# Performance work log

Hardware: AMD Instinct MI355X
Metric: run time of the kernel (lower is better)

## Reference

```python
import jax, jax.numpy as jnp
import numpy as np
from jax.ops import segment_sum

N_NODES = 100000

def setup_inputs() -> dict:
    key = jax.random.key(0)
    k1, k2, k3 = jax.random.split(key, 3)
    x = jax.random.normal(k1, (N_NODES, 128), dtype=jnp.float32)
    edge_weight = jax.random.uniform(k2, (3200000,), dtype=jnp.float32)
    edge_index = jax.random.randint(k3, (2, 3200000), 0, N_NODES, dtype=jnp.int64)
    return {"x": x, "edge_weight": edge_weight, "edge_index": edge_index}

def reference(x, edge_weight, edge_index):
    # GCNConv with weight forced to identity (in==out channels, no bias):
    # lin(x) == x, so the op is gcn_norm + scatter-add aggregation.
    n = x.shape[0]
    # add self loops with fill value 1.0 (improved=False)
    loop_idx = jnp.arange(n, dtype=edge_index.dtype)
    row = jnp.concatenate([edge_index[0], loop_idx])
    col = jnp.concatenate([edge_index[1], loop_idx])
    ew = jnp.concatenate([edge_weight, jnp.ones((n,), dtype=edge_weight.dtype)])
    # symmetric normalization: deg computed at target (col)
    deg = segment_sum(ew, col, num_segments=n)
    dinv = jnp.where(deg > 0, jax.lax.rsqrt(deg), 0.0)
    norm = dinv[row] * ew * dinv[col]
    # message = norm * x[src]; aggregate (sum) at target
    msgs = x[row] * norm[:, None]          # [E+N, d]
    out = segment_sum(msgs, col, num_segments=n)  # [N, d]
    return out
```

## Files before the change

kernel.cpp:

```cpp
#include <hip/hip_runtime.h>
#include <hip/hip_fp16.h>
#include <math.h>

#define FEAT      128
#define PITCH     72
#define CH        6144
#define K_EDGES   12
#define MAXBINS   512
#define CAP_MAX   9216
#define K2        18

__global__ void conv_xs_kernel(const float* __restrict__ x,
                               const float* __restrict__ dinv,
                               __half2* __restrict__ xs, int n4) {
    int i = blockIdx.x * blockDim.x + threadIdx.x;
    if (i >= n4) return;
    float s = dinv[i >> 5];
    float4 v = ((const float4*)x)[i];
    xs[2 * i]     = __floats2half2_rn(s * v.x, s * v.y);
    xs[2 * i + 1] = __floats2half2_rn(s * v.z, s * v.w);
}

__global__ __launch_bounds__(512) void p1_partition_kernel(
        const int* __restrict__ row,
        const int* __restrict__ col,
        const float* __restrict__ ew,
        int* __restrict__ bin_cursor,
        unsigned long long* __restrict__ binned,
        int E, int NBINS, int cap) {
    __shared__ unsigned long long stage[CH];
    __shared__ int hist[MAXBINS];
    __shared__ int lofs[MAXBINS];
    __shared__ int lcnt[MAXBINS];
    __shared__ int gbase[MAXBINS];
    __shared__ int scanbuf[MAXBINS];
    int tid = threadIdx.x;
    if (tid < MAXBINS) { hist[tid] = 0; lcnt[tid] = 0; }
    __syncthreads();

    int start = blockIdx.x * CH;
    int end   = start + CH; if (end > E) end = E;
    int total = end - start;

    unsigned long long ed[K_EDGES];
    int ebin[K_EDGES];
    #pragma unroll
    for (int k = 0; k < K_EDGES; k++) {
        int e = start + (k << 9) + tid;
        if (e < end) {
            int c = col[e];
            unsigned short wh = __half_as_ushort(__float2half_rn(ew[e]));
            ed[k] = ((unsigned long long)wh << 48)
                  | ((unsigned long long)((unsigned)row[e] & 0xFFFFFFu) << 24)
                  | (unsigned)(c & 0xFFFFFFu);
            ebin[k] = c >> 8;
            atomicAdd(&hist[ebin[k]], 1);
        } else {
            ebin[k] = -1;
        }
    }
    __syncthreads();

    int h = (tid < NBINS) ? hist[tid] : 0;
    scanbuf[tid] = h;
    __syncthreads();
    #pragma unroll
    for (int off = 1; off < MAXBINS; off <<= 1) {
        int t = (tid >= off) ? scanbuf[tid - off] : 0;
        __syncthreads();
        scanbuf[tid] += t;
        __syncthreads();
    }
    lofs[tid] = scanbuf[tid] - h;
    __syncthreads();

    #pragma unroll
    for (int k = 0; k < K_EDGES; k++) {
        if (ebin[k] >= 0) {
            int pos = lofs[ebin[k]] + atomicAdd(&lcnt[ebin[k]], 1);
            stage[pos] = ed[k];
        }
    }
    if (tid < NBINS)
        gbase[tid] = hist[tid] ? atomicAdd(&bin_cursor[tid], hist[tid]) : 0;
    __syncthreads();

    for (int i = tid; i < total; i += 512) {
        unsigned long long e = stage[i];
        int bin = (int)((e >> 8) & 0xFFFFu);
        int pos = gbase[bin] + (i - lofs[bin]);
        if (pos < cap) binned[(size_t)bin * cap + pos] = e;
    }
}

__global__ __launch_bounds__(512) void p2_build_kernel(
        const unsigned long long* __restrict__ binned,
        int* __restrict__ bin_cursor,
        unsigned long long* __restrict__ csr,
        float* __restrict__ dinv,
        int* __restrict__ countg,
        const float* __restrict__ x,
        __half2* __restrict__ xs,
        int N, int NBINS, int cap) {
    __shared__ unsigned long long stage[CAP_MAX];
    __shared__ float degf[256];
    __shared__ int cnt[256];
    __shared__ int pfx[256];
    __shared__ int lcnt[256];
    __shared__ float sdi[256];
    __shared__ int wsum[4];
    __shared__ int binBase_s;
    int tid = threadIdx.x;
    if (tid < 256) { degf[tid] = 0.0f; cnt[tid] = 0; lcnt[tid] = 0; }
    __syncthreads();

    int b = blockIdx.x;
    int nE = bin_cursor[b]; if (nE > cap) nE = cap;
    const unsigned long long* src = binned + (size_t)b * cap;
    int nodeBase = b << 8;

    unsigned long long ed[K2];
    #pragma unroll
    for (int k = 0; k < K2; k++) {
        int i = tid + (k << 9);
        if (i < nE) {
            unsigned long long p = src[i];
            int cl     = (int)(p & 255u);
            unsigned r = (unsigned)((p >> 24) & 0xFFFFFFu);
            float w = __half2float(__ushort_as_half((unsigned short)(p >> 48)));
            atomicAdd(&cnt[cl], 1);
            atomicAdd(&degf[cl], w);
            ed[k] = ((unsigned long long)__float_as_uint(w) << 32)
                  | ((unsigned)cl << 24) | r;
        }
    }
    if (tid == 0) binBase_s = atomicAdd(&bin_cursor[NBINS], nE);
    __syncthreads();

    if (tid < 256) {
        int w = tid >> 6, l = tid & 63;
        int v = cnt[tid];
        int inc = v;
        #pragma unroll
        for (int d = 1; d < 64; d <<= 1) {
            int t = __shfl_up(inc, d);
            if (l >= d) inc += t;
        }
        if (l == 63) wsum[w] = inc;
        pfx[tid] = inc - v;
    }
    __syncthreads();
    if (tid < 256) {
        int w = tid >> 6;
        int add = 0;
        for (int q = 0; q < w; q++) add += wsum[q];
        pfx[tid] += add;
    }
    __syncthreads();

    #pragma unroll
    for (int k = 0; k < K2; k++) {
        int i = tid + (k << 9);
        if (i < nE) {
            unsigned long long p = ed[k];
            int cl = (int)((p >> 24) & 255u);
            int slot = atomicAdd(&lcnt[cl], 1);
            stage[pfx[cl] + slot] = p & 0xFFFFFFFF00FFFFFFULL;
        }
    }
    __syncthreads();

    int binBase = binBase_s;
    for (int i = tid; i < nE; i += 512)
        csr[(size_t)binBase + i] = stage[i];
    if (tid < 256) {
        int node = nodeBase + tid;
        if (node < N) {
            float di = rsqrtf(1.0f + degf[tid]);
            sdi[tid] = di;
            dinv[node] = di;
            int c2 = cnt[tid]; if (c2 > 255) c2 = 255;
            countg[node] = (int)((((unsigned)(binBase + pfx[tid])) << 8) | (unsigned)c2);
        } else {
            sdi[tid] = 0.0f;
        }
    }
    __syncthreads();

    int nValid = N - nodeBase; if (nValid > 256) nValid = 256;
    if (nValid > 0) {
        int total4 = nValid << 5;
        for (int idx = tid; idx < total4; idx += 512) {
            int cl = idx >> 5;
            float s = sdi[cl];
            size_t g = ((size_t)(nodeBase + cl) << 5) + (idx & 31);
            float4 v = ((const float4*)x)[g];
            xs[2 * g]     = __floats2half2_rn(s * v.x, s * v.y);
            xs[2 * g + 1] = __floats2half2_rn(s * v.z, s * v.w);
        }
    }
}

#define GLD(q)  unsigned long long p##q = eb[wid][j + q];               \
                unsigned r##q = (unsigned)p##q;                          \
                float w##q = __uint_as_float((unsigned)(p##q >> 32));    \
                __half2 h##q = xs[(r##q << 6) | lane];
#define GFMA(q, acc)  { float2 v##q = __half22float2(h##q);              \
                acc.x = fmaf(w##q, v##q.x, acc.x);                       \
                acc.y = fmaf(w##q, v##q.y, acc.y); }

__global__ __launch_bounds__(256) void gather_xs_kernel(
        const __half2* __restrict__ xs,
        const float* __restrict__ dinv,
        const int* __restrict__ countg,
        const unsigned long long* __restrict__ csr,
        float* __restrict__ out, int nodeBase, int nEnd) {
    __shared__ unsigned long long eb[4][64];
    int wid  = threadIdx.x >> 6;
    int node = nodeBase + blockIdx.x * 4 + wid;
    int lane = threadIdx.x & 63;
    if (node >= nEnd) return;

    float di = dinv[node];
    unsigned c = (unsigned)countg[node];
    int cnt = (int)(c & 255u);
    const unsigned long long* b = csr + (c >> 8);

    unsigned long long e0 = (lane < cnt) ? b[lane] : 0ULL;
    eb[wid][lane] = e0;

    unsigned xbase = ((unsigned)node << 6) | (unsigned)lane;
    float2 xv = __half22float2(xs[xbase]);
    float2 a0 = xv;
    float2 a1 = {0.f, 0.f}, a2 = {0.f, 0.f}, a3 = {0.f, 0.f};

    int m = cnt < 64 ? cnt : 64;
    int j = 0;
    for (; j + 16 <= m; j += 16) {
        GLD(0)  GLD(1)  GLD(2)  GLD(3)  GLD(4)  GLD(5)  GLD(6)  GLD(7)
        GLD(8)  GLD(9)  GLD(10) GLD(11) GLD(12) GLD(13) GLD(14) GLD(15)
        GFMA(0, a0)  GFMA(1, a1)  GFMA(2, a2)  GFMA(3, a3)
        GFMA(4, a0)  GFMA(5, a1)  GFMA(6, a2)  GFMA(7, a3)
        GFMA(8, a0)  GFMA(9, a1)  GFMA(10, a2) GFMA(11, a3)
        GFMA(12, a0) GFMA(13, a1) GFMA(14, a2) GFMA(15, a3)
    }
    for (; j + 8 <= m; j += 8) {
        GLD(0)  GLD(1)  GLD(2)  GLD(3)  GLD(4)  GLD(5)  GLD(6)  GLD(7)
        GFMA(0, a0)  GFMA(1, a1)  GFMA(2, a2)  GFMA(3, a3)
        GFMA(4, a0)  GFMA(5, a1)  GFMA(6, a2)  GFMA(7, a3)
    }
    for (; j + 4 <= m; j += 4) {
        GLD(0)  GLD(1)  GLD(2)  GLD(3)
        GFMA(0, a0)  GFMA(1, a1)  GFMA(2, a2)  GFMA(3, a3)
    }
    for (; j < m; ++j) {
        GLD(0)
        GFMA(0, a0)
    }
    for (; j < cnt; ++j) {
        unsigned long long p0 = b[j];
        unsigned r0 = (unsigned)p0;
        float w0 = __uint_as_float((unsigned)(p0 >> 32));
        float2 v0 = __half22float2(xs[(r0 << 6) | lane]);
        a0.x = fmaf(w0, v0.x, a0.x);  a0.y = fmaf(w0, v0.y, a0.y);
    }
    float2 r;
    r.x = di * ((a0.x + a1.x) + (a2.x + a3.x));
    r.y = di * ((a0.y + a1.y) + (a2.y + a3.y));
    ((float2*)(out + (size_t)node * FEAT))[lane] = r;
}


__global__ void init_packed_kernel(unsigned long long* __restrict__ packed, int n) {
    int i = blockIdx.x * blockDim.x + threadIdx.x;
    if (i < n) packed[i] = (1ULL << 32);
}

__global__ void passA_kernel(const int* __restrict__ row,
                             const int* __restrict__ col,
                             const float* __restrict__ ew,
                             unsigned long long* __restrict__ packed,
                             unsigned long long* __restrict__ bucket, int E) {
    int e = blockIdx.x * blockDim.x + threadIdx.x;
    if (e >= E) return;
    int c = col[e], r = row[e];
    float w = ew[e];
    unsigned long long v = (1ULL << 40)
        | (unsigned long long)((double)w * 4294967296.0);
    unsigned long long old = atomicAdd(&packed[c], v);
    unsigned int slot = (unsigned int)(old >> 40);
    if (slot < PITCH)
        bucket[(size_t)c * PITCH + slot] =
            ((unsigned long long)__float_as_uint(w) << 32) | ((unsigned int)r & 0xFFFFFFu);
}

__global__ void make_dinv_count_kernel(const unsigned long long* __restrict__ packed,
                                       float* __restrict__ dinv,
                                       int* __restrict__ countg, int n) {
    int i = blockIdx.x * blockDim.x + threadIdx.x;
    if (i < n) {
        unsigned long long p = packed[i];
        unsigned long long frac = p & ((1ULL << 40) - 1);
        float d = (float)((double)frac * (1.0 / 4294967296.0));
        dinv[i] = rsqrtf(d);
        int c = (int)(p >> 40); if (c > PITCH) c = PITCH;
        countg[i] = (int)((((unsigned)i * (unsigned)PITCH) << 8) | (unsigned)c);
    }
}


__global__ void init_deg_kernel(float* __restrict__ deg, int n) {
    int i = blockIdx.x * blockDim.x + threadIdx.x;
    if (i < n) deg[i] = 1.0f;
}
__global__ void deg_accum_kernel(const int* __restrict__ col,
                                 const float* __restrict__ ew,
                                 float* __restrict__ deg, int E) {
    int e = blockIdx.x * blockDim.x + threadIdx.x;
    if (e < E) atomicAdd(&deg[col[e]], ew[e]);
}
__global__ void make_dinv_kernel(const float* __restrict__ deg,
                                 float* __restrict__ dinv, int n) {
    int i = blockIdx.x * blockDim.x + threadIdx.x;
    if (i < n) {
        float d = deg[i];
        dinv[i] = d > 0.0f ? rsqrtf(d) : 0.0f;
    }
}
__global__ void init_out_kernel(const float* __restrict__ x,
                                const float* __restrict__ dinv,
                                float* __restrict__ out, int n) {
    int idx = blockIdx.x * blockDim.x + threadIdx.x;
    int i = idx >> 5, lane = idx & 31;
    if (i >= n) return;
    float s = dinv[i] * dinv[i];
    float4 v = ((const float4*)(x + (size_t)i * FEAT))[lane];
    float4 r;
    r.x = s * v.x; r.y = s * v.y; r.z = s * v.z; r.w = s * v.w;
    ((float4*)(out + (size_t)i * FEAT))[lane] = r;
}
__global__ void scatter_kernel(const float* __restrict__ x,
                               const float* __restrict__ ew,
                               const int* __restrict__ row,
                               const int* __restrict__ col,
                               const float* __restrict__ dinv,
                               float* __restrict__ out, int E) {
    long long idx = (long long)blockIdx.x * blockDim.x + threadIdx.x;
    int e = (int)(idx >> 5), lane = (int)(idx & 31);
    if (e >= E) return;
    int r = row[e], c = col[e];
    float nrm = dinv[r] * ew[e] * dinv[c];
    float4 v = ((const float4*)(x + (size_t)r * FEAT))[lane];
    float* o = out + (size_t)c * FEAT + lane * 4;
    atomicAdd(o + 0, nrm * v.x);
    atomicAdd(o + 1, nrm * v.y);
    atomicAdd(o + 2, nrm * v.z);
    atomicAdd(o + 3, nrm * v.w);
}


static inline size_t align256(size_t v) { return (v + 255) & ~(size_t)255; }

extern "C" void kernel_launch(void* const* d_in, const int* in_sizes, int n_in,
                              void* d_out, int out_size, void* d_ws, size_t ws_size,
                              hipStream_t stream) {
    const float* x  = (const float*)d_in[0];
    const float* ew = (const float*)d_in[1];
    const int*   ei = (const int*)d_in[2];

    const int N = in_sizes[0] / FEAT;
    const int E = in_sizes[1];
    const int* row = ei;
    const int* col = ei + E;

    float* out = (float*)d_out;
    const int B = 256;
    char* w = (char*)d_ws;

    const int NBINS = (N + 255) >> 8;
    const int avg   = (E + NBINS - 1) / NBINS;
    int cap = avg + 8 * (int)sqrt((double)avg) + 64;
    if (cap > CAP_MAX) cap = CAP_MAX;

    size_t sz_csr    = align256((size_t)E * 8 + 256);
    size_t sz_bucket = align256((size_t)N * PITCH * 8);
    size_t sz_dinv   = align256((size_t)N * 4);
    size_t sz_count  = align256((size_t)N * 4);
    size_t sz_cursor = align256((size_t)(NBINS + 1) * 4);
    size_t sz_binned = align256((size_t)NBINS * (size_t)cap * 8);
    size_t sz_xs     = align256((size_t)N * FEAT * 2);

    size_t need_fast2 = sz_csr + sz_dinv + sz_count + sz_cursor + sz_binned + sz_xs;
    size_t need_fast1 = align256((size_t)N * 8) + sz_dinv + sz_count + sz_xs + sz_bucket;

    int n4 = N * FEAT / 4;

    if (ws_size >= need_fast2 && NBINS <= MAXBINS && N < (1 << 24) && E < (1 << 24)) {
        unsigned long long* csr = (unsigned long long*)w;     w += sz_csr;
        float* dinv   = (float*)w;                            w += sz_dinv;
        int*   countg = (int*)w;                              w += sz_count;
        int*   cursor = (int*)w;                              w += sz_cursor;
        unsigned long long* binned = (unsigned long long*)w;  w += sz_binned;
        __half2* xs = (__half2*)w;

        hipMemsetAsync(cursor, 0, (size_t)(NBINS + 1) * 4, stream);
        int p1b = (E + CH - 1) / CH;
        p1_partition_kernel<<<p1b, 512, 0, stream>>>(row, col, ew, cursor, binned,
                                                     E, NBINS, cap);
        p2_build_kernel<<<NBINS, 512, 0, stream>>>(binned, cursor, csr,
                                                   dinv, countg, x, xs, N, NBINS, cap);
        int q = ((N / 4) + 3) & ~3;
        for (int s4 = 0; s4 < 4; s4++) {
            int lo = q * s4;
            int hi = (s4 == 3) ? N : q * (s4 + 1);
            if (hi > lo)
                gather_xs_kernel<<<(hi - lo + 3) / 4, B, 0, stream>>>(
                    xs, dinv, countg, csr, out, lo, hi);
        }
    } else if (ws_size >= need_fast1 && N < (1 << 24) &&
               (size_t)N * PITCH < (size_t)(1 << 24)) {
        unsigned long long* packed = (unsigned long long*)w;  w += align256((size_t)N * 8);
        float*   dinv   = (float*)w;                          w += sz_dinv;
        int*     countg = (int*)w;                            w += sz_count;
        __half2* xs     = (__half2*)w;                        w += sz_xs;
        unsigned long long* bucket = (unsigned long long*)w;

        init_packed_kernel<<<(N + B - 1) / B, B, 0, stream>>>(packed, N);
        passA_kernel<<<(E + B - 1) / B, B, 0, stream>>>(row, col, ew, packed, bucket, E);
        make_dinv_count_kernel<<<(N + B - 1) / B, B, 0, stream>>>(packed, dinv, countg, N);
        conv_xs_kernel<<<(n4 + B - 1) / B, B, 0, stream>>>(x, dinv, xs, n4);
        gather_xs_kernel<<<(N + 3) / 4, B, 0, stream>>>(xs, dinv, countg, bucket, out, 0, N);
    } else {
        float* deg  = (float*)w;                  w += sz_dinv;
        float* dinv = (float*)w;
        init_deg_kernel<<<(N + B - 1) / B, B, 0, stream>>>(deg, N);
        deg_accum_kernel<<<(E + B - 1) / B, B, 0, stream>>>(col, ew, deg, E);
        make_dinv_kernel<<<(N + B - 1) / B, B, 0, stream>>>(deg, dinv, N);
        long long it = (long long)N * 32;
        init_out_kernel<<<(int)((it + B - 1) / B), B, 0, stream>>>(x, dinv, out, N);
        long long st = (long long)E * 32;
        scatter_kernel<<<(int)((st + B - 1) / B), B, 0, stream>>>(x, ew, row, col, dinv, out, E);
    }
}
```

Before: 303.7 us.

## Write CSR directly into padded per-bin slots and merge gather launches

The build kernel no longer stages edges in a 72 KB shared buffer and no longer compacts the CSR through a global atomic cursor. Each bin now writes straight into its own padded region at b*cap plus the per-node prefix, and the count/offset words are encoded against that padded layout. The cost is a second read of the binned input and scattered 8-byte global writes in place of coalesced copies, plus a larger workspace. The four partial gather launches are merged into a single launch over all nodes, removing launch overhead.

```diff
diff --git a/kernel.cpp b/kernel.cpp
--- a/kernel.cpp
+++ b/kernel.cpp
@@ -95,21 +95,19 @@
 
 __global__ __launch_bounds__(512) void p2_build_kernel(
         const unsigned long long* __restrict__ binned,
-        int* __restrict__ bin_cursor,
+        const int* __restrict__ bin_cursor,
         unsigned long long* __restrict__ csr,
         float* __restrict__ dinv,
         int* __restrict__ countg,
         const float* __restrict__ x,
         __half2* __restrict__ xs,
         int N, int NBINS, int cap) {
-    __shared__ unsigned long long stage[CAP_MAX];
     __shared__ float degf[256];
     __shared__ int cnt[256];
     __shared__ int pfx[256];
     __shared__ int lcnt[256];
     __shared__ float sdi[256];
     __shared__ int wsum[4];
-    __shared__ int binBase_s;
     int tid = threadIdx.x;
     if (tid < 256) { degf[tid] = 0.0f; cnt[tid] = 0; lcnt[tid] = 0; }
     __syncthreads();
@@ -119,22 +117,13 @@
     const unsigned long long* src = binned + (size_t)b * cap;
     int nodeBase = b << 8;
 
-    unsigned long long ed[K2];
-    #pragma unroll
-    for (int k = 0; k < K2; k++) {
-        int i = tid + (k << 9);
-        if (i < nE) {
-            unsigned long long p = src[i];
-            int cl     = (int)(p & 255u);
-            unsigned r = (unsigned)((p >> 24) & 0xFFFFFFu);
-            float w = __half2float(__ushort_as_half((unsigned short)(p >> 48)));
-            atomicAdd(&cnt[cl], 1);
-            atomicAdd(&degf[cl], w);
-            ed[k] = ((unsigned long long)__float_as_uint(w) << 32)
-                  | ((unsigned)cl << 24) | r;
-        }
-    }
-    if (tid == 0) binBase_s = atomicAdd(&bin_cursor[NBINS], nE);
+    for (int i = tid; i < nE; i += 512) {
+        unsigned long long p = src[i];
+        int cl = (int)(p & 255u);
+        float w = __half2float(__ushort_as_half((unsigned short)(p >> 48)));
+        atomicAdd(&cnt[cl], 1);
+        atomicAdd(&degf[cl], w);
+    }
     __syncthreads();
 
     if (tid < 256) {
@@ -154,38 +143,31 @@
         int w = tid >> 6;
         int add = 0;
         for (int q = 0; q < w; q++) add += wsum[q];
-        pfx[tid] += add;
-    }
-    __syncthreads();
-
-    #pragma unroll
-    for (int k = 0; k < K2; k++) {
-        int i = tid + (k << 9);
-        if (i < nE) {
-            unsigned long long p = ed[k];
-            int cl = (int)((p >> 24) & 255u);
-            int slot = atomicAdd(&lcnt[cl], 1);
-            stage[pfx[cl] + slot] = p & 0xFFFFFFFF00FFFFFFULL;
-        }
-    }
-    __syncthreads();
-
-    int binBase = binBase_s;
-    for (int i = tid; i < nE; i += 512)
-        csr[(size_t)binBase + i] = stage[i];
-    if (tid < 256) {
+        int p = pfx[tid] + add;
+        pfx[tid] = p;
         int node = nodeBase + tid;
         if (node < N) {
             float di = rsqrtf(1.0f + degf[tid]);
             sdi[tid] = di;
             dinv[node] = di;
             int c2 = cnt[tid]; if (c2 > 255) c2 = 255;
-            countg[node] = (int)((((unsigned)(binBase + pfx[tid])) << 8) | (unsigned)c2);
+            countg[node] = (int)((((unsigned)(b * cap + p)) << 8) | (unsigned)c2);
         } else {
             sdi[tid] = 0.0f;
         }
     }
     __syncthreads();
+
+    size_t base = (size_t)b * cap;
+    for (int i = tid; i < nE; i += 512) {
+        unsigned long long p = src[i];
+        int cl     = (int)(p & 255u);
+        unsigned r = (unsigned)((p >> 24) & 0xFFFFFFu);
+        float w = __half2float(__ushort_as_half((unsigned short)(p >> 48)));
+        int slot = atomicAdd(&lcnt[cl], 1);
+        csr[base + pfx[cl] + slot] =
+            ((unsigned long long)__float_as_uint(w) << 32) | r;
+    }
 
     int nValid = N - nodeBase; if (nValid > 256) nValid = 256;
     if (nValid > 0) {
@@ -382,41 +364,35 @@
     int cap = avg + 8 * (int)sqrt((double)avg) + 64;
     if (cap > CAP_MAX) cap = CAP_MAX;
 
-    size_t sz_csr    = align256((size_t)E * 8 + 256);
     size_t sz_bucket = align256((size_t)N * PITCH * 8);
     size_t sz_dinv   = align256((size_t)N * 4);
     size_t sz_count  = align256((size_t)N * 4);
-    size_t sz_cursor = align256((size_t)(NBINS + 1) * 4);
+    size_t sz_cursor = align256((size_t)NBINS * 4);
     size_t sz_binned = align256((size_t)NBINS * (size_t)cap * 8);
     size_t sz_xs     = align256((size_t)N * FEAT * 2);
 
-    size_t need_fast2 = sz_csr + sz_dinv + sz_count + sz_cursor + sz_binned + sz_xs;
+    size_t need_fast2 = sz_binned  + sz_dinv + sz_count + sz_cursor
+                      + sz_binned + sz_xs;
     size_t need_fast1 = align256((size_t)N * 8) + sz_dinv + sz_count + sz_xs + sz_bucket;
 
     int n4 = N * FEAT / 4;
 
     if (ws_size >= need_fast2 && NBINS <= MAXBINS && N < (1 << 24) && E < (1 << 24)) {
-        unsigned long long* csr = (unsigned long long*)w;     w += sz_csr;
+        unsigned long long* csr = (unsigned long long*)w;     w += sz_binned;
         float* dinv   = (float*)w;                            w += sz_dinv;
         int*   countg = (int*)w;                              w += sz_count;
         int*   cursor = (int*)w;                              w += sz_cursor;
         unsigned long long* binned = (unsigned long long*)w;  w += sz_binned;
         __half2* xs = (__half2*)w;
 
-        hipMemsetAsync(cursor, 0, (size_t)(NBINS + 1) * 4, stream);
+        hipMemsetAsync(cursor, 0, (size_t)NBINS * 4, stream);
         int p1b = (E + CH - 1) / CH;
         p1_partition_kernel<<<p1b, 512, 0, stream>>>(row, col, ew, cursor, binned,
                                                      E, NBINS, cap);
         p2_build_kernel<<<NBINS, 512, 0, stream>>>(binned, cursor, csr,
                                                    dinv, countg, x, xs, N, NBINS, cap);
-        int q = ((N / 4) + 3) & ~3;
-        for (int s4 = 0; s4 < 4; s4++) {
-            int lo = q * s4;
-            int hi = (s4 == 3) ? N : q * (s4 + 1);
-            if (hi > lo)
-                gather_xs_kernel<<<(hi - lo + 3) / 4, B, 0, stream>>>(
-                    xs, dinv, countg, csr, out, lo, hi);
-        }
+        gather_xs_kernel<<<(N + 3) / 4, B, 0, stream>>>(xs, dinv, countg, csr,
+                                                        out, 0, N);
     } else if (ws_size >= need_fast1 && N < (1 << 24) &&
                (size_t)N * PITCH < (size_t)(1 << 24)) {
         unsigned long long* packed = (unsigned long long*)w;  w += align256((size_t)N * 8);
```

Measured after the change: 315.5 us. 3.9% more time.
